# Kernel optimization log

Measured on AMD Instinct MI355X. Metric: run time of the kernel, lower is better.

Reference implementation:

```python
import jax, jax.numpy as jnp
import numpy as np

DIM = 2048
N_HEAD = 16
HEAD_DIM = DIM // N_HEAD


def setup_inputs() -> dict:
    key = jax.random.key(0)
    ks = jax.random.split(key, 7)
    B, N = 2, 2048
    s = 1.0 / np.sqrt(DIM)
    return {
        "x": jax.random.normal(ks[0], (B, N, DIM), dtype=jnp.float32),
        "Wq": jax.random.normal(ks[1], (DIM, DIM), dtype=jnp.float32) * s,
        "bq": jnp.zeros((DIM,), dtype=jnp.float32),
        "Wkv": jax.random.normal(ks[2], (DIM, 2 * HEAD_DIM), dtype=jnp.float32) * s,
        "bkv": jnp.zeros((2 * HEAD_DIM,), dtype=jnp.float32),
        "Wo": jax.random.normal(ks[3], (DIM, DIM), dtype=jnp.float32) * s,
        "bo": jnp.zeros((DIM,), dtype=jnp.float32),
    }


def reference(x, Wq, bq, Wkv, bkv, Wo, bo):
    B, N, D = x.shape
    # Q projection -> (B, H, N, hd)
    q = (x @ Wq + bq).reshape(B, N, N_HEAD, HEAD_DIM).transpose(0, 2, 1, 3)
    # shared single-head K/V (kv = x, self-attention path)
    kvp = x @ Wkv + bkv  # (B, M, 2*hd)
    k, v = kvp[..., :HEAD_DIM], kvp[..., HEAD_DIM:]  # (B, M, hd) each
    scale = 1.0 / np.sqrt(HEAD_DIM).astype(np.float32)
    # broadcast shared K over heads without materializing expanded K/V
    scores = jnp.einsum("bhnd,bmd->bhnm", q, k) * scale  # (B, H, N, M)
    attn = jax.nn.softmax(scores, axis=-1)
    out = jnp.einsum("bhnm,bmd->bhnd", attn, v)  # (B, H, N, hd)
    out = out.transpose(0, 2, 1, 3).reshape(B, N, D)
    return out @ Wo + bo
```

## Files before the change

### kernel.cpp

```cpp
#include <hip/hip_runtime.h>
#include <math.h>

using bf16x8 = __attribute__((ext_vector_type(8))) short;
using f32x4  = __attribute__((ext_vector_type(4))) float;
using f32x16 = __attribute__((ext_vector_type(16))) float;
using u16x4  = __attribute__((ext_vector_type(4))) unsigned short;
using u32x4  = __attribute__((ext_vector_type(4))) unsigned int;

#define DIMSZ 2048
#define NSEQ  2048
#define BATCH 2
#define NHEAD 16
#define HD    128

__device__ __forceinline__ unsigned short f2bf(float x) {
    unsigned int u = __builtin_bit_cast(unsigned int, x);
    unsigned int r = (u + 0x7FFFu + ((u >> 16) & 1u)) >> 16;
    return (unsigned short)r;
}

__device__ __forceinline__ unsigned int cvtpk_bf16(float lo, float hi) {
    unsigned int r;
    asm("v_cvt_pk_bf16_f32 %0, %1, %2" : "=v"(r) : "v"(lo), "v"(hi));
    return r;
}

__device__ __forceinline__ void gload_lds16(const unsigned short* g, unsigned short* l) {
    __builtin_amdgcn_global_load_lds(
        (const __attribute__((address_space(1))) unsigned int*)g,
        (__attribute__((address_space(3))) unsigned int*)l, 16, 0, 0);
}

__global__ void k_cast_bf16(const float* __restrict__ in, unsigned short* __restrict__ out, int n4) {
    int i = blockIdx.x * blockDim.x + threadIdx.x;
    if (i >= n4) return;
    f32x4 v = *(const f32x4*)(in + (size_t)i * 4);
    u16x4 o;
#pragma unroll
    for (int j = 0; j < 4; j++) o[j] = f2bf(v[j]);
    *(u16x4*)(out + (size_t)i * 4) = o;
}

__global__ void k_transpose_all(const float* __restrict__ Wq, const float* __restrict__ Wkv,
                                const float* __restrict__ Wo, unsigned short* __restrict__ wqkvt,
                                unsigned short* __restrict__ wot, float sc) {
    __shared__ float t[32][33];
    const int ct = blockIdx.x;
    const int k0 = blockIdx.y * 32;
    const float* src;
    unsigned short* dst;
    float scale;
    int N, n0;
    if (ct < 64)      { src = Wq;  dst = wqkvt;                       scale = sc;   N = 2048; n0 = ct * 32; }
    else if (ct < 72) { src = Wkv; dst = wqkvt + (size_t)2048 * 2048; scale = 1.0f; N = 256;  n0 = (ct - 64) * 32; }
    else              { src = Wo;  dst = wot;                         scale = 1.0f; N = 2048; n0 = (ct - 72) * 32; }
    const int tx = threadIdx.x, ty = threadIdx.y;
#pragma unroll
    for (int i = 0; i < 32; i += 8) t[ty + i][tx] = src[(size_t)(k0 + ty + i) * N + n0 + tx];
    __syncthreads();
#pragma unroll
    for (int i = 0; i < 32; i += 8)
        dst[(size_t)(n0 + ty + i) * 2048 + k0 + tx] = f2bf(t[tx][ty + i] * scale);
}

__global__ void k_transpose_v(const unsigned short* __restrict__ kvp, unsigned short* __restrict__ vt) {
    __shared__ unsigned short t[32][33];
    int n0 = blockIdx.x * 32, d0 = blockIdx.y * 32, b = blockIdx.z;
    int tx = threadIdx.x, ty = threadIdx.y;
#pragma unroll
    for (int i = 0; i < 32; i += 8)
        t[ty + i][tx] = kvp[(size_t)(b * NSEQ + n0 + ty + i) * 256 + 128 + d0 + tx];
    __syncthreads();
#pragma unroll
    for (int i = 0; i < 32; i += 8)
        vt[(size_t)(b * HD + d0 + ty + i) * NSEQ + n0 + tx] = t[tx][ty + i];
}

__device__ __forceinline__ void xcd_tile(int nbx, int& bx, int& by) {
    int wg = ((int)blockIdx.x & 7) * ((int)gridDim.x >> 3) + ((int)blockIdx.x >> 3);
    bx = wg % nbx;
    by = wg / nbx;
}

__global__ __launch_bounds__(256, 2)
void k_gemm_qkv(const unsigned short* __restrict__ A, const unsigned short* __restrict__ Bt,
                const float* __restrict__ bq, float bscale, const float* __restrict__ bkv,
                unsigned short* __restrict__ qout, unsigned short* __restrict__ kvout,
                int M, int K, int nbx) {
    __shared__ unsigned short As[2][128 * 32];
    __shared__ unsigned short Bs[2][128 * 32];
    const int tid = threadIdx.x;
    const int wid = tid >> 6;
    const int lane = tid & 63;
    const int g = lane >> 4, cc = lane & 15;
    const int wr = wid >> 1, wc = wid & 1;
    int bx, by;
    xcd_tile(nbx, bx, by);
    const size_t m0 = (size_t)by * 128;
    const size_t n0 = (size_t)bx * 128;

    f32x4 acc[4][4] = {};

    const int srow = wid * 32 + (lane >> 2);
    const int sch = lane & 3;
    const unsigned short* gA = A + (m0 + srow) * (size_t)K + sch * 8;
    const unsigned short* gB = Bt + (n0 + srow) * (size_t)K + sch * 8;
    const int lo = wid * 32 * 32;

    auto STAGE = [&](int buf, int k0) {
        gload_lds16(gA + k0, &As[buf][lo]);
        gload_lds16(gA + 16 * (size_t)K + k0, &As[buf][lo + 16 * 32]);
        gload_lds16(gB + k0, &Bs[buf][lo]);
        gload_lds16(gB + 16 * (size_t)K + k0, &Bs[buf][lo + 16 * 32]);
    };

    STAGE(0, 0);
    __syncthreads();
    int cur = 0;
    for (int k0 = 0; k0 < K; k0 += 32) {
        if (k0 + 32 < K) STAGE(cur ^ 1, k0 + 32);
        bf16x8 af[4], bfr[4];
#pragma unroll
        for (int mi = 0; mi < 4; mi++) af[mi] = *(const bf16x8*)(&As[cur][(wr * 64 + mi * 16 + cc) * 32 + g * 8]);
#pragma unroll
        for (int ni = 0; ni < 4; ni++) bfr[ni] = *(const bf16x8*)(&Bs[cur][(wc * 64 + ni * 16 + cc) * 32 + g * 8]);
#pragma unroll
        for (int mi = 0; mi < 4; mi++)
#pragma unroll
            for (int ni = 0; ni < 4; ni++)
                acc[mi][ni] = __builtin_amdgcn_mfma_f32_16x16x32_bf16(af[mi], bfr[ni], acc[mi][ni], 0, 0, 0);
        __syncthreads();
        cur ^= 1;
    }

    const bool isQ = (n0 < 2048);
    const int colg = (int)n0 + wc * 64 + cc;
    const int col0 = isQ ? colg : colg - 2048;
    const int ostride = isQ ? 2048 : 256;
    unsigned short* outp = isQ ? qout : kvout;
    float bia[4];
#pragma unroll
    for (int ni = 0; ni < 4; ni++)
        bia[ni] = isQ ? bq[col0 + ni * 16] * bscale : bkv[col0 + ni * 16];
#pragma unroll
    for (int mi = 0; mi < 4; mi++) {
        size_t row = m0 + wr * 64 + mi * 16 + g * 4;
#pragma unroll
        for (int ni = 0; ni < 4; ni++)
#pragma unroll
            for (int r = 0; r < 4; r++)
                outp[(row + r) * ostride + col0 + ni * 16] = f2bf(acc[mi][ni][r] + bia[ni]);
    }
}

__global__ __launch_bounds__(256, 2)
void k_gemm_bt_f32(const unsigned short* __restrict__ A, const unsigned short* __restrict__ Bt,
                   const float* __restrict__ bias, float* __restrict__ Cout,
                   int M, int N, int K, int nbx) {
    __shared__ unsigned short As[2][128 * 32];
    __shared__ unsigned short Bs[2][128 * 32];
    const int tid = threadIdx.x;
    const int wid = tid >> 6;
    const int lane = tid & 63;
    const int g = lane >> 4, cc = lane & 15;
    const int wr = wid >> 1, wc = wid & 1;
    int bx, by;
    xcd_tile(nbx, bx, by);
    const size_t m0 = (size_t)by * 128;
    const size_t n0 = (size_t)bx * 128;

    f32x4 acc[4][4] = {};

    const int srow = wid * 32 + (lane >> 2);
    const int sch = lane & 3;
    const unsigned short* gA = A + (m0 + srow) * (size_t)K + sch * 8;
    const unsigned short* gB = Bt + (n0 + srow) * (size_t)K + sch * 8;
    const int lo = wid * 32 * 32;

    auto STAGE = [&](int buf, int k0) {
        gload_lds16(gA + k0, &As[buf][lo]);
        gload_lds16(gA + 16 * (size_t)K + k0, &As[buf][lo + 16 * 32]);
        gload_lds16(gB + k0, &Bs[buf][lo]);
        gload_lds16(gB + 16 * (size_t)K + k0, &Bs[buf][lo + 16 * 32]);
    };

    STAGE(0, 0);
    __syncthreads();
    int cur = 0;
    for (int k0 = 0; k0 < K; k0 += 32) {
        if (k0 + 32 < K) STAGE(cur ^ 1, k0 + 32);
        bf16x8 af[4], bfr[4];
#pragma unroll
        for (int mi = 0; mi < 4; mi++) af[mi] = *(const bf16x8*)(&As[cur][(wr * 64 + mi * 16 + cc) * 32 + g * 8]);
#pragma unroll
        for (int ni = 0; ni < 4; ni++) bfr[ni] = *(const bf16x8*)(&Bs[cur][(wc * 64 + ni * 16 + cc) * 32 + g * 8]);
#pragma unroll
        for (int mi = 0; mi < 4; mi++)
#pragma unroll
            for (int ni = 0; ni < 4; ni++)
                acc[mi][ni] = __builtin_amdgcn_mfma_f32_16x16x32_bf16(af[mi], bfr[ni], acc[mi][ni], 0, 0, 0);
        __syncthreads();
        cur ^= 1;
    }

    const int col0 = (int)n0 + wc * 64 + cc;
    float bia[4];
#pragma unroll
    for (int ni = 0; ni < 4; ni++) bia[ni] = bias[col0 + ni * 16];
#pragma unroll
    for (int mi = 0; mi < 4; mi++) {
        size_t row = m0 + wr * 64 + mi * 16 + g * 4;
#pragma unroll
        for (int ni = 0; ni < 4; ni++)
#pragma unroll
            for (int r = 0; r < 4; r++)
                Cout[(row + r) * N + col0 + ni * 16] = acc[mi][ni][r] + bia[ni];
    }
}

__global__ __launch_bounds__(256, 2)
void k_attn(const unsigned short* __restrict__ q, const unsigned short* __restrict__ kvp,
            const unsigned short* __restrict__ vt, unsigned short* __restrict__ out) {
    __shared__ unsigned char Kb[2][16384];
    __shared__ unsigned char Vb[2][16384];

    const int b = blockIdx.z, h = blockIdx.y, qt = blockIdx.x;
    const int tid = threadIdx.x, w = tid >> 6, lane = tid & 63;
    const int q32 = lane & 31, hi = lane >> 5;

    const int qrow = qt * 128 + w * 32 + q32;
    const unsigned short* qp = q + (size_t)(b * NSEQ + qrow) * DIMSZ + h * HD + hi * 8;
    bf16x8 qf[8];
#pragma unroll
    for (int dc = 0; dc < 8; dc++) qf[dc] = *(const bf16x8*)(qp + dc * 16);

    const char* kvpc = (const char*)kvp;
    const char* vtc  = (const char*)vt;
    size_t srcK[4], srcV[4];
#pragma unroll
    for (int c = 0; c < 4; c++) {
        unsigned int o = (tid + c * 256) * 16;
        unsigned int krow = o >> 8, kcol = o & 255;
        srcK[c] = (size_t)(b * NSEQ + krow) * 512 + (kcol ^ (((krow >> 1) & 15) << 4));
        unsigned int vrow = o >> 7, vcol = o & 127;
        srcV[c] = (size_t)(b * HD + vrow) * 4096 + (vcol ^ (((vrow >> 2) & 7) << 4));
    }

    auto STAGE = [&](int buf, int t) {
        size_t kb_ = (size_t)t * 32768;
        size_t vb_ = (size_t)t * 128;
#pragma unroll
        for (int c = 0; c < 4; c++) {
            gload_lds16((const unsigned short*)(kvpc + srcK[c] + kb_),
                        (unsigned short*)(Kb[buf] + (w * 64 + c * 256) * 16));
            gload_lds16((const unsigned short*)(vtc + srcV[c] + vb_),
                        (unsigned short*)(Vb[buf] + (w * 64 + c * 256) * 16));
        }
    };

    f32x16 o0 = {}, o1 = {}, o2 = {}, o3 = {};
    float l_run = 0.0f;
    const unsigned int swK = ((q32 >> 1) & 15) << 4;
    const unsigned int swV = ((q32 >> 2) & 7) << 4;

#define PROC_KT(S, KTB)                                                               \
    {                                                                                 \
        float pz[16];                                                                 \
        _Pragma("unroll") for (int r = 0; r < 16; r++) {                              \
            pz[r] = __builtin_amdgcn_exp2f(S[r]);                                     \
            l_run += pz[r];                                                           \
        }                                                                             \
        _Pragma("unroll") for (int kc = 0; kc < 2; kc++) {                            \
            unsigned int own01 = cvtpk_bf16(pz[kc * 8 + 0], pz[kc * 8 + 1]);          \
            unsigned int own23 = cvtpk_bf16(pz[kc * 8 + 2], pz[kc * 8 + 3]);          \
            unsigned int own45 = cvtpk_bf16(pz[kc * 8 + 4], pz[kc * 8 + 5]);          \
            unsigned int own67 = cvtpk_bf16(pz[kc * 8 + 6], pz[kc * 8 + 7]);          \
            unsigned int send_a = hi ? own01 : own45;                                 \
            unsigned int send_b = hi ? own23 : own67;                                 \
            unsigned int got_a = (unsigned int)__shfl_xor((int)send_a, 32, 64);       \
            unsigned int got_b = (unsigned int)__shfl_xor((int)send_b, 32, 64);       \
            u32x4 awv;                                                                \
            awv[0] = hi ? got_a : own01;                                              \
            awv[1] = hi ? got_b : own23;                                              \
            awv[2] = hi ? own45 : got_a;                                              \
            awv[3] = hi ? own67 : got_b;                                              \
            bf16x8 pa = __builtin_bit_cast(bf16x8, awv);                              \
            const unsigned int kbo = (KTB) + kc * 32 + hi * 16;                       \
            bf16x8 vf0 = *(const bf16x8*)(Vc + (q32 + 0) * 128 + (kbo ^ swV));        \
            bf16x8 vf1 = *(const bf16x8*)(Vc + (q32 + 32) * 128 + (kbo ^ swV));       \
            bf16x8 vf2 = *(const bf16x8*)(Vc + (q32 + 64) * 128 + (kbo ^ swV));       \
            bf16x8 vf3 = *(const bf16x8*)(Vc + (q32 + 96) * 128 + (kbo ^ swV));       \
            __builtin_amdgcn_s_setprio(1);                                            \
            o0 = __builtin_amdgcn_mfma_f32_32x32x16_bf16(pa, vf0, o0, 0, 0, 0);       \
            o1 = __builtin_amdgcn_mfma_f32_32x32x16_bf16(pa, vf1, o1, 0, 0, 0);       \
            o2 = __builtin_amdgcn_mfma_f32_32x32x16_bf16(pa, vf2, o2, 0, 0, 0);       \
            o3 = __builtin_amdgcn_mfma_f32_32x32x16_bf16(pa, vf3, o3, 0, 0, 0);       \
            __builtin_amdgcn_s_setprio(0);                                            \
        }                                                                             \
    }

    STAGE(0, 0);
    __syncthreads();

    for (int t = 0; t < NSEQ / 64; t++) {
        const int cur = t & 1;
        if (t < NSEQ / 64 - 1) STAGE(cur ^ 1, t + 1);

        const unsigned char* Kc = Kb[cur];
        const unsigned char* Vc = Vb[cur];

        f32x16 s0 = {}, s1 = {};
#pragma unroll
        for (int dc = 0; dc < 8; dc++) {
            const unsigned int db = dc * 32 + hi * 16;
            bf16x8 kf0 = *(const bf16x8*)(Kc + q32 * 256 + (db ^ swK));
            bf16x8 kf1 = *(const bf16x8*)(Kc + (q32 + 32) * 256 + (db ^ swK));
            __builtin_amdgcn_s_setprio(1);
            s0 = __builtin_amdgcn_mfma_f32_32x32x16_bf16(kf0, qf[dc], s0, 0, 0, 0);
            s1 = __builtin_amdgcn_mfma_f32_32x32x16_bf16(kf1, qf[dc], s1, 0, 0, 0);
            __builtin_amdgcn_s_setprio(0);
        }

        PROC_KT(s0, 0)
        PROC_KT(s1, 64)

        __syncthreads();
    }
#undef PROC_KT

    l_run += __shfl_xor(l_run, 32, 64);
    float* Lp = (float*)(Kb[0] + w * 128);
    if (hi == 0) Lp[q32] = l_run;

    float rinv[16];
#pragma unroll
    for (int r = 0; r < 16; r++) {
        int qloc = (r & 3) + 8 * (r >> 2) + 4 * hi;
        rinv[r] = 1.0f / Lp[qloc];
    }

    unsigned short* op = out + (size_t)(b * NSEQ + qt * 128 + w * 32) * DIMSZ + h * HD + q32;
#pragma unroll
    for (int r = 0; r < 16; r++) {
        int qloc = (r & 3) + 8 * (r >> 2) + 4 * hi;
        op[(size_t)qloc * DIMSZ + 0]  = f2bf(o0[r] * rinv[r]);
        op[(size_t)qloc * DIMSZ + 32] = f2bf(o1[r] * rinv[r]);
        op[(size_t)qloc * DIMSZ + 64] = f2bf(o2[r] * rinv[r]);
        op[(size_t)qloc * DIMSZ + 96] = f2bf(o3[r] * rinv[r]);
    }
}

extern "C" void kernel_launch(void* const* d_in, const int* in_sizes, int n_in,
                              void* d_out, int out_size, void* d_ws, size_t ws_size,
                              hipStream_t stream) {
    const float* x   = (const float*)d_in[0];
    const float* Wq  = (const float*)d_in[1];
    const float* bq  = (const float*)d_in[2];
    const float* Wkv = (const float*)d_in[3];
    const float* bkv = (const float*)d_in[4];
    const float* Wo  = (const float*)d_in[5];
    const float* bo  = (const float*)d_in[6];

    char* w = (char*)d_ws;
    unsigned short* xb    = (unsigned short*)(w);
    unsigned short* wqkvt = (unsigned short*)(w + 16777216);
    unsigned short* wot   = (unsigned short*)(w + 26214400);
    unsigned short* qb    = (unsigned short*)(w + 34603008);
    unsigned short* kvpb  = (unsigned short*)(w + 51380224);
    unsigned short* vtb   = (unsigned short*)(w + 53477376);
    unsigned short* aob   = xb;

    const float sc = 0.08838834764831845f * 1.4426950408889634f;

    k_cast_bf16<<<dim3((BATCH * NSEQ * DIMSZ / 4 + 255) / 256), dim3(256), 0, stream>>>(
        x, xb, BATCH * NSEQ * DIMSZ / 4);
    k_transpose_all<<<dim3(136, 64), dim3(32, 8), 0, stream>>>(Wq, Wkv, Wo, wqkvt, wot, sc);

    k_gemm_qkv<<<dim3((2304 / 128) * (BATCH * NSEQ / 128)), dim3(256), 0, stream>>>(
        xb, wqkvt, bq, sc, bkv, qb, kvpb, BATCH * NSEQ, DIMSZ, 2304 / 128);
    k_transpose_v<<<dim3(NSEQ / 32, HD / 32, BATCH), dim3(32, 8), 0, stream>>>(kvpb, vtb);
    k_attn<<<dim3(NSEQ / 128, NHEAD, BATCH), dim3(256), 0, stream>>>(qb, kvpb, vtb, aob);
    k_gemm_bt_f32<<<dim3((DIMSZ / 128) * (BATCH * NSEQ / 128)), dim3(256), 0, stream>>>(
        aob, wot, bo, (float*)d_out, BATCH * NSEQ, DIMSZ, DIMSZ, DIMSZ / 128);
}
```

Measured before the change: 204.3 us.

## Use 256x128 GEMM tiles with 512 threads and triple-buffered LDS pipeline

Both GEMM kernels move to 512-thread blocks that each compute a 256x128 output tile. The K loop now uses a three-stage LDS ring with explicit vmcnt waits and a single barrier per iteration, replacing double buffering with two syncthreads. The goal is to keep two loads in flight to hide global-load latency and to reuse each B tile across more rows. In exchange, LDS use per block grows, and the launch bound of 4 blocks per CU of 512 threads may limit registers and occupancy.

```diff
diff --git a/kernel.cpp b/kernel.cpp
--- a/kernel.cpp
+++ b/kernel.cpp
@@ -82,140 +82,91 @@
     by = wg / nbx;
 }
 
-__global__ __launch_bounds__(256, 2)
+#define GEMM_BODY(EPILOGUE)                                                                    \
+    __shared__ unsigned short As[3][256 * 32];                                                 \
+    __shared__ unsigned short Bs[3][128 * 32];                                                 \
+    const int tid = threadIdx.x;                                                               \
+    const int wid = tid >> 6;                                                                  \
+    const int lane = tid & 63;                                                                 \
+    const int g = lane >> 4, cc = lane & 15;                                                   \
+    const int wm = wid >> 1, wn = wid & 1;                                                     \
+    int bx, by;                                                                                \
+    xcd_tile(nbx, bx, by);                                                                     \
+    const size_t m0 = (size_t)by * 256;                                                        \
+    const size_t n0 = (size_t)bx * 128;                                                        \
+    f32x4 acc[4][4] = {};                                                                      \
+               \
+    const unsigned short* gA0 = A + (m0 + (tid >> 2)) * (size_t)K + (tid & 3) * 8;             \
+    const unsigned short* gA1 = A + (m0 + 128 + (tid >> 2)) * (size_t)K + (tid & 3) * 8;       \
+    const unsigned short* gB  = Bt + (n0 + (tid >> 2)) * (size_t)K + (tid & 3) * 8;            \
+    const int NT = K / 32;                                                                     \
+    auto STAGE = [&](int buf, int k0) {                                                        \
+        gload_lds16(gA0 + k0, &As[buf][wid * 512]);                                            \
+        gload_lds16(gA1 + k0, &As[buf][4096 + wid * 512]);                                     \
+        gload_lds16(gB + k0, &Bs[buf][wid * 512]);                                             \
+    };                                                                                         \
+    STAGE(0, 0);                                                                               \
+    STAGE(1, 32);                                                                              \
+    for (int t = 0; t < NT; ++t) {                                                             \
+        if (t < NT - 1)                                                                        \
+            asm volatile("s_waitcnt vmcnt(3)" ::: "memory");                                   \
+        else                                                                                   \
+            asm volatile("s_waitcnt vmcnt(0)" ::: "memory");                                   \
+        __builtin_amdgcn_s_barrier();                                                          \
+        __builtin_amdgcn_sched_barrier(0);                                                     \
+        if (t + 2 < NT) STAGE((t + 2) % 3, (t + 2) * 32);                                      \
+        const unsigned short* Ac = &As[t % 3][0];                                              \
+        const unsigned short* Bc = &Bs[t % 3][0];                                              \
+        bf16x8 af[4], bfr[4];                                                                  \
+        _Pragma("unroll") for (int mi = 0; mi < 4; mi++)                                       \
+            af[mi] = *(const bf16x8*)(Ac + (wm * 64 + mi * 16 + cc) * 32 + g * 8);             \
+        _Pragma("unroll") for (int ni = 0; ni < 4; ni++)                                       \
+            bfr[ni] = *(const bf16x8*)(Bc + (wn * 64 + ni * 16 + cc) * 32 + g * 8);            \
+        _Pragma("unroll") for (int mi = 0; mi < 4; mi++)                                       \
+            _Pragma("unroll") for (int ni = 0; ni < 4; ni++)                                   \
+                acc[mi][ni] = __builtin_amdgcn_mfma_f32_16x16x32_bf16(af[mi], bfr[ni],         \
+                                                                      acc[mi][ni], 0, 0, 0);  \
+    }                                                                                          \
+    EPILOGUE
+
+__global__ __launch_bounds__(512, 4)
 void k_gemm_qkv(const unsigned short* __restrict__ A, const unsigned short* __restrict__ Bt,
                 const float* __restrict__ bq, float bscale, const float* __restrict__ bkv,
                 unsigned short* __restrict__ qout, unsigned short* __restrict__ kvout,
                 int M, int K, int nbx) {
-    __shared__ unsigned short As[2][128 * 32];
-    __shared__ unsigned short Bs[2][128 * 32];
-    const int tid = threadIdx.x;
-    const int wid = tid >> 6;
-    const int lane = tid & 63;
-    const int g = lane >> 4, cc = lane & 15;
-    const int wr = wid >> 1, wc = wid & 1;
-    int bx, by;
-    xcd_tile(nbx, bx, by);
-    const size_t m0 = (size_t)by * 128;
-    const size_t n0 = (size_t)bx * 128;
-
-    f32x4 acc[4][4] = {};
-
-    const int srow = wid * 32 + (lane >> 2);
-    const int sch = lane & 3;
-    const unsigned short* gA = A + (m0 + srow) * (size_t)K + sch * 8;
-    const unsigned short* gB = Bt + (n0 + srow) * (size_t)K + sch * 8;
-    const int lo = wid * 32 * 32;
-
-    auto STAGE = [&](int buf, int k0) {
-        gload_lds16(gA + k0, &As[buf][lo]);
-        gload_lds16(gA + 16 * (size_t)K + k0, &As[buf][lo + 16 * 32]);
-        gload_lds16(gB + k0, &Bs[buf][lo]);
-        gload_lds16(gB + 16 * (size_t)K + k0, &Bs[buf][lo + 16 * 32]);
-    };
-
-    STAGE(0, 0);
-    __syncthreads();
-    int cur = 0;
-    for (int k0 = 0; k0 < K; k0 += 32) {
-        if (k0 + 32 < K) STAGE(cur ^ 1, k0 + 32);
-        bf16x8 af[4], bfr[4];
-#pragma unroll
-        for (int mi = 0; mi < 4; mi++) af[mi] = *(const bf16x8*)(&As[cur][(wr * 64 + mi * 16 + cc) * 32 + g * 8]);
-#pragma unroll
-        for (int ni = 0; ni < 4; ni++) bfr[ni] = *(const bf16x8*)(&Bs[cur][(wc * 64 + ni * 16 + cc) * 32 + g * 8]);
-#pragma unroll
-        for (int mi = 0; mi < 4; mi++)
-#pragma unroll
-            for (int ni = 0; ni < 4; ni++)
-                acc[mi][ni] = __builtin_amdgcn_mfma_f32_16x16x32_bf16(af[mi], bfr[ni], acc[mi][ni], 0, 0, 0);
-        __syncthreads();
-        cur ^= 1;
-    }
-
-    const bool isQ = (n0 < 2048);
-    const int colg = (int)n0 + wc * 64 + cc;
-    const int col0 = isQ ? colg : colg - 2048;
-    const int ostride = isQ ? 2048 : 256;
-    unsigned short* outp = isQ ? qout : kvout;
-    float bia[4];
-#pragma unroll
-    for (int ni = 0; ni < 4; ni++)
-        bia[ni] = isQ ? bq[col0 + ni * 16] * bscale : bkv[col0 + ni * 16];
-#pragma unroll
-    for (int mi = 0; mi < 4; mi++) {
-        size_t row = m0 + wr * 64 + mi * 16 + g * 4;
-#pragma unroll
-        for (int ni = 0; ni < 4; ni++)
-#pragma unroll
-            for (int r = 0; r < 4; r++)
-                outp[(row + r) * ostride + col0 + ni * 16] = f2bf(acc[mi][ni][r] + bia[ni]);
-    }
-}
-
-__global__ __launch_bounds__(256, 2)
+    GEMM_BODY({
+        const bool isQ = (n0 < 2048);
+        const int colg = (int)n0 + wn * 64 + cc;
+        const int col0 = isQ ? colg : colg - 2048;
+        const int ostride = isQ ? 2048 : 256;
+        unsigned short* outp = isQ ? qout : kvout;
+        float bia[4];
+        _Pragma("unroll") for (int ni = 0; ni < 4; ni++)
+            bia[ni] = isQ ? bq[col0 + ni * 16] * bscale : bkv[col0 + ni * 16];
+        _Pragma("unroll") for (int mi = 0; mi < 4; mi++) {
+            size_t row = m0 + wm * 64 + mi * 16 + g * 4;
+            _Pragma("unroll") for (int ni = 0; ni < 4; ni++)
+                _Pragma("unroll") for (int r = 0; r < 4; r++)
+                    outp[(row + r) * ostride + col0 + ni * 16] = f2bf(acc[mi][ni][r] + bia[ni]);
+        }
+    })
+}
+
+__global__ __launch_bounds__(512, 4)
 void k_gemm_bt_f32(const unsigned short* __restrict__ A, const unsigned short* __restrict__ Bt,
                    const float* __restrict__ bias, float* __restrict__ Cout,
                    int M, int N, int K, int nbx) {
-    __shared__ unsigned short As[2][128 * 32];
-    __shared__ unsigned short Bs[2][128 * 32];
-    const int tid = threadIdx.x;
-    const int wid = tid >> 6;
-    const int lane = tid & 63;
-    const int g = lane >> 4, cc = lane & 15;
-    const int wr = wid >> 1, wc = wid & 1;
-    int bx, by;
-    xcd_tile(nbx, bx, by);
-    const size_t m0 = (size_t)by * 128;
-    const size_t n0 = (size_t)bx * 128;
-
-    f32x4 acc[4][4] = {};
-
-    const int srow = wid * 32 + (lane >> 2);
-    const int sch = lane & 3;
-    const unsigned short* gA = A + (m0 + srow) * (size_t)K + sch * 8;
-    const unsigned short* gB = Bt + (n0 + srow) * (size_t)K + sch * 8;
-    const int lo = wid * 32 * 32;
-
-    auto STAGE = [&](int buf, int k0) {
-        gload_lds16(gA + k0, &As[buf][lo]);
-        gload_lds16(gA + 16 * (size_t)K + k0, &As[buf][lo + 16 * 32]);
-        gload_lds16(gB + k0, &Bs[buf][lo]);
-        gload_lds16(gB + 16 * (size_t)K + k0, &Bs[buf][lo + 16 * 32]);
-    };
-
-    STAGE(0, 0);
-    __syncthreads();
-    int cur = 0;
-    for (int k0 = 0; k0 < K; k0 += 32) {
-        if (k0 + 32 < K) STAGE(cur ^ 1, k0 + 32);
-        bf16x8 af[4], bfr[4];
-#pragma unroll
-        for (int mi = 0; mi < 4; mi++) af[mi] = *(const bf16x8*)(&As[cur][(wr * 64 + mi * 16 + cc) * 32 + g * 8]);
-#pragma unroll
-        for (int ni = 0; ni < 4; ni++) bfr[ni] = *(const bf16x8*)(&Bs[cur][(wc * 64 + ni * 16 + cc) * 32 + g * 8]);
-#pragma unroll
-        for (int mi = 0; mi < 4; mi++)
-#pragma unroll
-            for (int ni = 0; ni < 4; ni++)
-                acc[mi][ni] = __builtin_amdgcn_mfma_f32_16x16x32_bf16(af[mi], bfr[ni], acc[mi][ni], 0, 0, 0);
-        __syncthreads();
-        cur ^= 1;
-    }
-
-    const int col0 = (int)n0 + wc * 64 + cc;
-    float bia[4];
-#pragma unroll
-    for (int ni = 0; ni < 4; ni++) bia[ni] = bias[col0 + ni * 16];
-#pragma unroll
-    for (int mi = 0; mi < 4; mi++) {
-        size_t row = m0 + wr * 64 + mi * 16 + g * 4;
-#pragma unroll
-        for (int ni = 0; ni < 4; ni++)
-#pragma unroll
-            for (int r = 0; r < 4; r++)
-                Cout[(row + r) * N + col0 + ni * 16] = acc[mi][ni][r] + bia[ni];
-    }
+    GEMM_BODY({
+        const int col0 = (int)n0 + wn * 64 + cc;
+        float bia[4];
+        _Pragma("unroll") for (int ni = 0; ni < 4; ni++) bia[ni] = bias[col0 + ni * 16];
+        _Pragma("unroll") for (int mi = 0; mi < 4; mi++) {
+            size_t row = m0 + wm * 64 + mi * 16 + g * 4;
+            _Pragma("unroll") for (int ni = 0; ni < 4; ni++)
+                _Pragma("unroll") for (int r = 0; r < 4; r++)
+                    Cout[(row + r) * N + col0 + ni * 16] = acc[mi][ni][r] + bia[ni];
+        }
+    })
 }
 
 __global__ __launch_bounds__(256, 2)
@@ -376,10 +327,10 @@
         x, xb, BATCH * NSEQ * DIMSZ / 4);
     k_transpose_all<<<dim3(136, 64), dim3(32, 8), 0, stream>>>(Wq, Wkv, Wo, wqkvt, wot, sc);
 
-    k_gemm_qkv<<<dim3((2304 / 128) * (BATCH * NSEQ / 128)), dim3(256), 0, stream>>>(
+    k_gemm_qkv<<<dim3((BATCH * NSEQ / 256) * (2304 / 128)), dim3(512), 0, stream>>>(
         xb, wqkvt, bq, sc, bkv, qb, kvpb, BATCH * NSEQ, DIMSZ, 2304 / 128);
     k_transpose_v<<<dim3(NSEQ / 32, HD / 32, BATCH), dim3(32, 8), 0, stream>>>(kvpb, vtb);
     k_attn<<<dim3(NSEQ / 128, NHEAD, BATCH), dim3(256), 0, stream>>>(qb, kvpb, vtb, aob);
-    k_gemm_bt_f32<<<dim3((DIMSZ / 128) * (BATCH * NSEQ / 128)), dim3(256), 0, stream>>>(
+    k_gemm_bt_f32<<<dim3((BATCH * NSEQ / 256) * (DIMSZ / 128)), dim3(512), 0, stream>>>(
         aob, wot, bo, (float*)d_out, BATCH * NSEQ, DIMSZ, DIMSZ, DIMSZ / 128);
 }
```

After: 224.1 us. 9.7% more time.
